# Kernel tuning notes

Measured on AMD Instinct MI355X. Metric: run time of the kernel, lower is better.

Reference implementation:

```python
import jax, jax.numpy as jnp
import numpy as np

Q7_MAX = 127.0  # int8 symmetric quant range
EPS = 1e-8


def setup_inputs() -> dict:
    key = jax.random.key(0)
    k0, k1, k2, k3 = jax.random.split(key, 4)
    tokens, d_in, d_out = 4096, 4096, 6144  # 32*128 + 8*128 + 8*128
    x = jax.random.normal(k0, (tokens, d_in), dtype=jnp.float32)
    # pre-quantized int8 weight [out_features, in_features]
    weight = jax.random.randint(k1, (d_out, d_in), -128, 128, dtype=jnp.int8)
    # per-output-channel dequant scale [out_features, 1]
    scale = jax.random.uniform(k2, (d_out, 1), dtype=jnp.float32, minval=1e-3, maxval=1e-2)
    bias = jax.random.normal(k3, (d_out,), dtype=jnp.float32) * 0.01
    return {"x": x, "weight": weight, "scale": scale, "bias": bias}


def reference(x, weight, scale, bias):
    # dynamic per-token symmetric int8 quantization of activations
    amax = jnp.max(jnp.abs(x), axis=-1, keepdims=True)          # [T, 1]
    s_x = jnp.maximum(amax, EPS) / Q7_MAX                        # per-token scale
    x_q = jnp.clip(jnp.round(x / s_x), -128.0, 127.0).astype(jnp.int8)
    acc = jnp.matmul(x_q.astype(jnp.int32), weight.astype(jnp.int32).T)
    # fused dequant: per-token act scale * per-channel weight scale, plus bias
    out = acc.astype(jnp.float32) * s_x * scale.T + bias
    return out
```

## Files before the change

kernel.cpp:

```cpp
#include <hip/hip_runtime.h>
#include <stdint.h>
#include <stddef.h>

typedef __attribute__((ext_vector_type(4))) int i32x4;

#define AS1q __attribute__((address_space(1)))
#define AS3q __attribute__((address_space(3)))

__device__ __forceinline__ void gload16(const void* g, void* l) {
    __builtin_amdgcn_global_load_lds((const AS1q uint32_t*)g, (AS3q uint32_t*)l, 16, 0, 0);
}

#define VMCNT0()  asm volatile("s_waitcnt vmcnt(0)" ::: "memory")
#define BARRIER() asm volatile("s_barrier" ::: "memory")
#define SB()      __builtin_amdgcn_sched_barrier(0)
#define SP1()     __builtin_amdgcn_s_setprio(1)
#define SP0()     __builtin_amdgcn_s_setprio(0)
#define MFMAI8(a, b, c) __builtin_amdgcn_mfma_i32_16x16x64_i8(a, b, c, 0, 0, 0)

#define EPSQ 1e-8f

__global__ __launch_bounds__(256) void quant4096(
    const float* __restrict__ x, int8_t* __restrict__ xq, float* __restrict__ sx)
{
    constexpr int K = 4096;
    const int t = blockIdx.x;
    const int tid = threadIdx.x;
    const float4* row4 = (const float4*)(x + (size_t)t * K);
    float4 v0 = row4[0 * 256 + tid];
    float4 v1 = row4[1 * 256 + tid];
    float4 v2 = row4[2 * 256 + tid];
    float4 v3 = row4[3 * 256 + tid];
    auto mx4 = [](float4 a) {
        return fmaxf(fmaxf(fabsf(a.x), fabsf(a.y)), fmaxf(fabsf(a.z), fabsf(a.w)));
    };
    float am = fmaxf(fmaxf(mx4(v0), mx4(v1)), fmaxf(mx4(v2), mx4(v3)));
    #pragma unroll
    for (int off = 32; off > 0; off >>= 1)
        am = fmaxf(am, __shfl_xor(am, off, 64));
    __shared__ float wmax[4];
    if ((tid & 63) == 0) wmax[tid >> 6] = am;
    __syncthreads();
    float r = fmaxf(fmaxf(wmax[0], wmax[1]), fmaxf(wmax[2], wmax[3]));
    const float s = fmaxf(r, EPSQ) / 127.0f;
    if (tid == 0) sx[t] = s;
    int* qrow = (int*)(xq + (size_t)t * K);
    auto pack = [&](float4 a) {
        int q0 = (int)fminf(fmaxf(rintf(a.x / s), -128.f), 127.f);
        int q1 = (int)fminf(fmaxf(rintf(a.y / s), -128.f), 127.f);
        int q2 = (int)fminf(fmaxf(rintf(a.z / s), -128.f), 127.f);
        int q3 = (int)fminf(fmaxf(rintf(a.w / s), -128.f), 127.f);
        return (q0 & 255) | ((q1 & 255) << 8) | ((q2 & 255) << 16) | ((q3 & 255) << 24);
    };
    qrow[0 * 256 + tid] = pack(v0);
    qrow[1 * 256 + tid] = pack(v1);
    qrow[2 * 256 + tid] = pack(v2);
    qrow[3 * 256 + tid] = pack(v3);
}

__global__ __launch_bounds__(256) void quant_any(
    const float* __restrict__ x, int8_t* __restrict__ xq, float* __restrict__ sx, int K)
{
    const int t = blockIdx.x;
    const int tid = threadIdx.x;
    const float* row = x + (size_t)t * K;
    float am = 0.f;
    for (int i = tid; i < K; i += 256) am = fmaxf(am, fabsf(row[i]));
    #pragma unroll
    for (int off = 32; off > 0; off >>= 1)
        am = fmaxf(am, __shfl_xor(am, off, 64));
    __shared__ float wmax[4];
    if ((tid & 63) == 0) wmax[tid >> 6] = am;
    __syncthreads();
    float r = fmaxf(fmaxf(wmax[0], wmax[1]), fmaxf(wmax[2], wmax[3]));
    const float s = fmaxf(r, EPSQ) / 127.0f;
    if (tid == 0) sx[t] = s;
    int8_t* qrow = xq + (size_t)t * K;
    for (int i = tid; i < K; i += 256) {
        float q = fminf(fmaxf(rintf(row[i] / s), -128.f), 127.f);
        qrow[i] = (int8_t)(int)q;
    }
}

__global__ __launch_bounds__(256) void pack_w(
    const int* __restrict__ w32, int8_t* __restrict__ w8, long long n4)
{
    const long long stride = (long long)gridDim.x * 256;
    for (long long i = (long long)blockIdx.x * 256 + threadIdx.x; i < n4; i += stride) {
        int4 v = ((const int4*)w32)[i];
        ((int*)w8)[i] = (v.x & 255) | ((v.y & 255) << 8) | ((v.z & 255) << 16) | ((v.w & 255) << 24);
    }
}

__global__ __launch_bounds__(512, 2) void gemm_i8(
    const int8_t* __restrict__ xq, const int8_t* __restrict__ w,
    const float* __restrict__ sx, const float* __restrict__ scale,
    const float* __restrict__ bias, float* __restrict__ out,
    int M, int N, int K)
{
    __shared__ __align__(16) uint8_t lds[2][57344];
    const int tid  = threadIdx.x;
    const int lane = tid & 63;
    const int wv   = tid >> 6;
    const int wr   = wv >> 2, wc = wv & 3;

    const int nwg = gridDim.x;
    const int q8 = nwg >> 3, r8 = nwg & 7;
    const int xcd = blockIdx.x & 7, idx8 = blockIdx.x >> 3;
    const int wg = (xcd < r8 ? xcd * (q8 + 1) : r8 * (q8 + 1) + (xcd - r8) * q8) + idx8;

    const int NBM = M >> 8;
    const int bm = wg % NBM;
    const int bn = wg / NBM;
    const int brow = bm << 8, bcol = bn * 192;

    const int8_t* srcA[4];
    #pragma unroll
    for (int e = 0; e < 4; ++e) {
        int half = e >> 1;
        int li = (e & 1) * 512 + tid;
        int R  = li >> 3;
        int xx = ((li & 7) << 4) ^ ((R & 7) << 4);
        srcA[e] = xq + (size_t)(brow + ((R << 1) | (xx >> 6))) * K + half * 64 + (xx & 63);
    }
    const int8_t* srcB[3];
    #pragma unroll
    for (int e = 0; e < 3; ++e) {
        int li = e * 512 + tid;
        int halfB = (li >= 768) ? 1 : 0;
        int lw = li - halfB * 768;
        int R  = lw >> 3;
        int xx = ((li & 7) << 4) ^ ((R & 7) << 4);
        srcB[e] = w + (size_t)(bcol + ((R << 1) | (xx >> 6))) * K + halfB * 64 + (xx & 63);
    }

    int offA[8], offB[3];
    #pragma unroll
    for (int m = 0; m < 8; ++m) {
        int r  = wr * 128 + m * 16 + (lane & 15);
        int R  = r >> 1;
        int x  = (((r & 1) << 6) | (lane & 48)) ^ ((R & 7) << 4);
        offA[m] = R * 128 + x;
    }
    #pragma unroll
    for (int n = 0; n < 3; ++n) {
        int r  = wc * 48 + n * 16 + (lane & 15);
        int R  = r >> 1;
        int x  = (((r & 1) << 6) | (lane & 48)) ^ ((R & 7) << 4);
        offB[n] = R * 128 + x;
    }

    i32x4 acc[8][3] = {};

#define STAGE(NB, TT) do { const size_t ko = (size_t)(TT) << 7;      \
        gload16(srcA[0] + ko, &lds[NB][        wv * 1024]);          \
        gload16(srcA[1] + ko, &lds[NB][ 8192 + wv * 1024]);          \
        gload16(srcA[2] + ko, &lds[NB][16384 + wv * 1024]);          \
        gload16(srcA[3] + ko, &lds[NB][24576 + wv * 1024]);          \
        gload16(srcB[0] + ko, &lds[NB][32768 + wv * 1024]);          \
        gload16(srcB[1] + ko, &lds[NB][40960 + wv * 1024]);          \
        gload16(srcB[2] + ko, &lds[NB][49152 + wv * 1024]); } while (0)

#define RA(BUF, HH, V, MM) V = *(const i32x4*)(&lds[BUF][(HH) * 16384 + offA[MM]])
#define RB(BUF, HH, V, NN) V = *(const i32x4*)(&lds[BUF][32768 + (HH) * 12288 + offB[NN]])

#define TILE(BUF, TT, DOSTAGE) do {                                           \
        i32x4 a0,a1,a2,a3,a4,a5,a6,a7,b0,b1,b2;                               \
        i32x4 c0,c1,c2,c3,c4,c5,c6,c7,d0,d1,d2;                               \
        VMCNT0(); BARRIER(); SB();                                            \
        RA(BUF,0,a0,0); RA(BUF,0,a1,1); RB(BUF,0,b0,0); RB(BUF,0,b1,1); SB(); \
        RA(BUF,0,a2,2); RA(BUF,0,a3,3); RB(BUF,0,b2,2); SB();                 \
        RA(BUF,0,a4,4); RA(BUF,0,a5,5); RA(BUF,0,a6,6); RA(BUF,0,a7,7); SB(); \
        if (DOSTAGE) { STAGE(BUF ^ 1, (TT) + 1); }                            \
        SB();                                                                 \
        SP1();                                                                \
        acc[0][0]=MFMAI8(a0,b0,acc[0][0]); acc[1][0]=MFMAI8(a1,b0,acc[1][0]); \
        acc[0][1]=MFMAI8(a0,b1,acc[0][1]); acc[1][1]=MFMAI8(a1,b1,acc[1][1]); \
        SP0(); SB();                                                          \
        RA(BUF,1,c0,0); RA(BUF,1,c1,1); RB(BUF,1,d0,0); RB(BUF,1,d1,1); SB(); \
        SP1();                                                                \
        acc[0][2]=MFMAI8(a0,b2,acc[0][2]); acc[1][2]=MFMAI8(a1,b2,acc[1][2]); \
        acc[2][0]=MFMAI8(a2,b0,acc[2][0]); acc[3][0]=MFMAI8(a3,b0,acc[3][0]); \
        acc[2][1]=MFMAI8(a2,b1,acc[2][1]); acc[3][1]=MFMAI8(a3,b1,acc[3][1]); \
        acc[2][2]=MFMAI8(a2,b2,acc[2][2]); acc[3][2]=MFMAI8(a3,b2,acc[3][2]); \
        SP0(); SB();                                                          \
        RA(BUF,1,c2,2); RA(BUF,1,c3,3); RB(BUF,1,d2,2); SB();                 \
        SP1();                                                                \
        acc[4][0]=MFMAI8(a4,b0,acc[4][0]); acc[5][0]=MFMAI8(a5,b0,acc[5][0]); \
        acc[6][0]=MFMAI8(a6,b0,acc[6][0]); acc[7][0]=MFMAI8(a7,b0,acc[7][0]); \
        acc[4][1]=MFMAI8(a4,b1,acc[4][1]); acc[5][1]=MFMAI8(a5,b1,acc[5][1]); \
        acc[6][1]=MFMAI8(a6,b1,acc[6][1]); acc[7][1]=MFMAI8(a7,b1,acc[7][1]); \
        acc[4][2]=MFMAI8(a4,b2,acc[4][2]); acc[5][2]=MFMAI8(a5,b2,acc[5][2]); \
        acc[6][2]=MFMAI8(a6,b2,acc[6][2]); acc[7][2]=MFMAI8(a7,b2,acc[7][2]); \
        SP0(); SB();                                                          \
        RA(BUF,1,c4,4); RA(BUF,1,c5,5); RA(BUF,1,c6,6); RA(BUF,1,c7,7); SB(); \
        SP1();                                                                \
        acc[0][0]=MFMAI8(c0,d0,acc[0][0]); acc[1][0]=MFMAI8(c1,d0,acc[1][0]); \
        acc[0][1]=MFMAI8(c0,d1,acc[0][1]); acc[1][1]=MFMAI8(c1,d1,acc[1][1]); \
        acc[0][2]=MFMAI8(c0,d2,acc[0][2]); acc[1][2]=MFMAI8(c1,d2,acc[1][2]); \
        acc[2][0]=MFMAI8(c2,d0,acc[2][0]); acc[3][0]=MFMAI8(c3,d0,acc[3][0]); \
        acc[2][1]=MFMAI8(c2,d1,acc[2][1]); acc[3][1]=MFMAI8(c3,d1,acc[3][1]); \
        acc[2][2]=MFMAI8(c2,d2,acc[2][2]); acc[3][2]=MFMAI8(c3,d2,acc[3][2]); \
        acc[4][0]=MFMAI8(c4,d0,acc[4][0]); acc[5][0]=MFMAI8(c5,d0,acc[5][0]); \
        acc[6][0]=MFMAI8(c6,d0,acc[6][0]); acc[7][0]=MFMAI8(c7,d0,acc[7][0]); \
        acc[4][1]=MFMAI8(c4,d1,acc[4][1]); acc[5][1]=MFMAI8(c5,d1,acc[5][1]); \
        acc[6][1]=MFMAI8(c6,d1,acc[6][1]); acc[7][1]=MFMAI8(c7,d1,acc[7][1]); \
        acc[4][2]=MFMAI8(c4,d2,acc[4][2]); acc[5][2]=MFMAI8(c5,d2,acc[5][2]); \
        acc[6][2]=MFMAI8(c6,d2,acc[6][2]); acc[7][2]=MFMAI8(c7,d2,acc[7][2]); \
        SP0(); SB();                                                          \
    } while (0)

    const int NT = K >> 7;
    STAGE(0, 0);
    for (int t = 0; t < NT - 2; t += 2) {
        TILE(0, t,     true);
        TILE(1, t + 1, true);
    }
    TILE(0, NT - 2, true);
    TILE(1, NT - 1, false);

    const int orow = brow + wr * 128;
    const int ocol = bcol + wc * 48;
    float sxv[8][4];
    #pragma unroll
    for (int m = 0; m < 8; ++m)
        #pragma unroll
        for (int j = 0; j < 4; ++j)
            sxv[m][j] = sx[orow + m * 16 + ((lane >> 4) << 2) + j];
    #pragma unroll
    for (int n = 0; n < 3; ++n) {
        const int col = ocol + n * 16 + (lane & 15);
        const float sc = scale[col];
        const float bi = bias[col];
        #pragma unroll
        for (int m = 0; m < 8; ++m) {
            const int rb = orow + m * 16 + ((lane >> 4) << 2);
            #pragma unroll
            for (int j = 0; j < 4; ++j)
                out[(size_t)(rb + j) * N + col] = (float)acc[m][n][j] * sxv[m][j] * sc + bi;
        }
    }
}

extern "C" void kernel_launch(void* const* d_in, const int* in_sizes, int n_in,
                              void* d_out, int out_size, void* d_ws, size_t ws_size,
                              hipStream_t stream) {
    const float* x     = (const float*)d_in[0];
    const int*   w32   = (const int*)d_in[1];
    const float* scale = (const float*)d_in[2];
    const float* bias  = (const float*)d_in[3];
    float* out = (float*)d_out;

    const int N = in_sizes[2];
    const int K = in_sizes[1] / N;
    const int M = in_sizes[0] / K;

    int8_t* xqbuf = (int8_t*)d_ws;
    int8_t* wqbuf = (int8_t*)d_ws + (size_t)M * K;
    float*  sxbuf = (float*)((uint8_t*)d_ws + (size_t)M * K + (size_t)N * K);

    if (K == 4096)
        quant4096<<<M, 256, 0, stream>>>(x, xqbuf, sxbuf);
    else
        quant_any<<<M, 256, 0, stream>>>(x, xqbuf, sxbuf, K);

    pack_w<<<2048, 256, 0, stream>>>(w32, wqbuf, (long long)N * K / 4);

    const int nwg = (M / 256) * (N / 192);
    gemm_i8<<<nwg, 512, 0, stream>>>(xqbuf, wqbuf, sxbuf, scale, bias, out, M, N, K);
}
```

Before: 142.1 us.

## Triple-buffer A tiles and use partial vmcnt waits to deepen the prefetch

Splits the shared LDS buffer into separate A and B regions: A gets three slots, B keeps two. Each iteration waits with vmcnt(4) instead of vmcnt(0), then issues the B load for the next tile and the A load two tiles ahead, both before the LDS reads of the current tile. The aim is to hide more global-load latency behind the MFMA work and avoid draining every outstanding load at each barrier. In exchange, LDS use per block rises to about 144 KB, and the pipeline prologue and epilogue get more special cases.

```diff
diff --git a/kernel.cpp b/kernel.cpp
--- a/kernel.cpp
+++ b/kernel.cpp
@@ -11,6 +11,7 @@
     __builtin_amdgcn_global_load_lds((const AS1q uint32_t*)g, (AS3q uint32_t*)l, 16, 0, 0);
 }
 
+#define VMCNT4()  asm volatile("s_waitcnt vmcnt(4)" ::: "memory")
 #define VMCNT0()  asm volatile("s_waitcnt vmcnt(0)" ::: "memory")
 #define BARRIER() asm volatile("s_barrier" ::: "memory")
 #define SB()      __builtin_amdgcn_sched_barrier(0)
@@ -98,7 +99,8 @@
     const float* __restrict__ bias, float* __restrict__ out,
     int M, int N, int K)
 {
-    __shared__ __align__(16) uint8_t lds[2][57344];
+    __shared__ __align__(16) uint8_t ldsA[3][32768];
+    __shared__ __align__(16) uint8_t ldsB[2][24576];
     const int tid  = threadIdx.x;
     const int lane = tid & 63;
     const int wv   = tid >> 6;
@@ -152,39 +154,37 @@
 
     i32x4 acc[8][3] = {};
 
-#define STAGE(NB, TT) do { const size_t ko = (size_t)(TT) << 7;      \
-        gload16(srcA[0] + ko, &lds[NB][        wv * 1024]);          \
-        gload16(srcA[1] + ko, &lds[NB][ 8192 + wv * 1024]);          \
-        gload16(srcA[2] + ko, &lds[NB][16384 + wv * 1024]);          \
-        gload16(srcA[3] + ko, &lds[NB][24576 + wv * 1024]);          \
-        gload16(srcB[0] + ko, &lds[NB][32768 + wv * 1024]);          \
-        gload16(srcB[1] + ko, &lds[NB][40960 + wv * 1024]);          \
-        gload16(srcB[2] + ko, &lds[NB][49152 + wv * 1024]); } while (0)
-
-#define RA(BUF, HH, V, MM) V = *(const i32x4*)(&lds[BUF][(HH) * 16384 + offA[MM]])
-#define RB(BUF, HH, V, NN) V = *(const i32x4*)(&lds[BUF][32768 + (HH) * 12288 + offB[NN]])
-
-#define TILE(BUF, TT, DOSTAGE) do {                                           \
+#define STAGE_A(DST, TT) do { const size_t ko = (size_t)(TT) << 7;   \
+        gload16(srcA[0] + ko, (DST) +         wv * 1024);            \
+        gload16(srcA[1] + ko, (DST) +  8192 + wv * 1024);            \
+        gload16(srcA[2] + ko, (DST) + 16384 + wv * 1024);            \
+        gload16(srcA[3] + ko, (DST) + 24576 + wv * 1024); } while (0)
+#define STAGE_B(DST, TT) do { const size_t ko = (size_t)(TT) << 7;   \
+        gload16(srcB[0] + ko, (DST) +         wv * 1024);            \
+        gload16(srcB[1] + ko, (DST) +  8192 + wv * 1024);            \
+        gload16(srcB[2] + ko, (DST) + 16384 + wv * 1024); } while (0)
+
+#define RA(BA, HH, V, MM) V = *(const i32x4*)((BA) + (HH) * 16384 + offA[MM])
+#define RB(BB, HH, V, NN) V = *(const i32x4*)((BB) + (HH) * 12288 + offB[NN])
+
+#define TILE_BODY(BA, BB) do {                                                \
         i32x4 a0,a1,a2,a3,a4,a5,a6,a7,b0,b1,b2;                               \
         i32x4 c0,c1,c2,c3,c4,c5,c6,c7,d0,d1,d2;                               \
-        VMCNT0(); BARRIER(); SB();                                            \
-        RA(BUF,0,a0,0); RA(BUF,0,a1,1); RB(BUF,0,b0,0); RB(BUF,0,b1,1); SB(); \
-        RA(BUF,0,a2,2); RA(BUF,0,a3,3); RB(BUF,0,b2,2); SB();                 \
-        RA(BUF,0,a4,4); RA(BUF,0,a5,5); RA(BUF,0,a6,6); RA(BUF,0,a7,7); SB(); \
-        if (DOSTAGE) { STAGE(BUF ^ 1, (TT) + 1); }                            \
-        SB();                                                                 \
+        RA(BA,0,a0,0); RA(BA,0,a1,1); RB(BB,0,b0,0); RB(BB,0,b1,1); SB();     \
+        RA(BA,0,a2,2); RA(BA,0,a3,3); RB(BB,0,b2,2); SB();                    \
+        RA(BA,0,a4,4); RA(BA,0,a5,5); RA(BA,0,a6,6); RA(BA,0,a7,7); SB();     \
         SP1();                                                                \
         acc[0][0]=MFMAI8(a0,b0,acc[0][0]); acc[1][0]=MFMAI8(a1,b0,acc[1][0]); \
         acc[0][1]=MFMAI8(a0,b1,acc[0][1]); acc[1][1]=MFMAI8(a1,b1,acc[1][1]); \
         SP0(); SB();                                                          \
-        RA(BUF,1,c0,0); RA(BUF,1,c1,1); RB(BUF,1,d0,0); RB(BUF,1,d1,1); SB(); \
+        RA(BA,1,c0,0); RA(BA,1,c1,1); RB(BB,1,d0,0); RB(BB,1,d1,1); SB();     \
         SP1();                                                                \
         acc[0][2]=MFMAI8(a0,b2,acc[0][2]); acc[1][2]=MFMAI8(a1,b2,acc[1][2]); \
         acc[2][0]=MFMAI8(a2,b0,acc[2][0]); acc[3][0]=MFMAI8(a3,b0,acc[3][0]); \
         acc[2][1]=MFMAI8(a2,b1,acc[2][1]); acc[3][1]=MFMAI8(a3,b1,acc[3][1]); \
         acc[2][2]=MFMAI8(a2,b2,acc[2][2]); acc[3][2]=MFMAI8(a3,b2,acc[3][2]); \
         SP0(); SB();                                                          \
-        RA(BUF,1,c2,2); RA(BUF,1,c3,3); RB(BUF,1,d2,2); SB();                 \
+        RA(BA,1,c2,2); RA(BA,1,c3,3); RB(BB,1,d2,2); SB();                    \
         SP1();                                                                \
         acc[4][0]=MFMAI8(a4,b0,acc[4][0]); acc[5][0]=MFMAI8(a5,b0,acc[5][0]); \
         acc[6][0]=MFMAI8(a6,b0,acc[6][0]); acc[7][0]=MFMAI8(a7,b0,acc[7][0]); \
@@ -193,7 +193,7 @@
         acc[4][2]=MFMAI8(a4,b2,acc[4][2]); acc[5][2]=MFMAI8(a5,b2,acc[5][2]); \
         acc[6][2]=MFMAI8(a6,b2,acc[6][2]); acc[7][2]=MFMAI8(a7,b2,acc[7][2]); \
         SP0(); SB();                                                          \
-        RA(BUF,1,c4,4); RA(BUF,1,c5,5); RA(BUF,1,c6,6); RA(BUF,1,c7,7); SB(); \
+        RA(BA,1,c4,4); RA(BA,1,c5,5); RA(BA,1,c6,6); RA(BA,1,c7,7); SB();     \
         SP1();                                                                \
         acc[0][0]=MFMAI8(c0,d0,acc[0][0]); acc[1][0]=MFMAI8(c1,d0,acc[1][0]); \
         acc[0][1]=MFMAI8(c0,d1,acc[0][1]); acc[1][1]=MFMAI8(c1,d1,acc[1][1]); \
@@ -211,13 +211,37 @@
     } while (0)
 
     const int NT = K >> 7;
-    STAGE(0, 0);
-    for (int t = 0; t < NT - 2; t += 2) {
-        TILE(0, t,     true);
-        TILE(1, t + 1, true);
-    }
-    TILE(0, NT - 2, true);
-    TILE(1, NT - 1, false);
+    STAGE_A(&ldsA[0][0], 0);
+    STAGE_B(&ldsB[0][0], 0);
+    STAGE_A(&ldsA[1][0], 1);
+
+    int ia = 0;
+    for (int t = 0; t < NT - 2; ++t) {
+        uint8_t* bA = &ldsA[ia][0];
+        uint8_t* bB = &ldsB[t & 1][0];
+        int ia2 = ia + 2; if (ia2 >= 3) ia2 -= 3;
+        VMCNT4(); BARRIER(); SB();
+        STAGE_B(&ldsB[(t & 1) ^ 1][0], t + 1);
+        STAGE_A(&ldsA[ia2][0], t + 2);
+        SB();
+        TILE_BODY(bA, bB);
+        ia = (ia == 2) ? 0 : ia + 1;
+    }
+    {
+        uint8_t* bA = &ldsA[ia][0];
+        uint8_t* bB = &ldsB[(NT - 2) & 1][0];
+        VMCNT4(); BARRIER(); SB();
+        STAGE_B(&ldsB[(NT - 1) & 1][0], NT - 1);
+        SB();
+        TILE_BODY(bA, bB);
+        ia = (ia == 2) ? 0 : ia + 1;
+    }
+    {
+        uint8_t* bA = &ldsA[ia][0];
+        uint8_t* bB = &ldsB[(NT - 1) & 1][0];
+        VMCNT0(); BARRIER(); SB();
+        TILE_BODY(bA, bB);
+    }
 
     const int orow = brow + wr * 128;
     const int ocol = bcol + wc * 48;
```

Measured after the change: 176.0 us. 23.8% more time.

## Switch GEMM inner loop to 32x32x32 int8 MFMA with 4x2 wave grid

Applied to the files above, without the earlier changes.

Replaces the 16x16x64 int8 MFMA with the 32x32x32 variant and changes the wave layout from 2x4 to 4x2. Each wave now computes a 64x96 sub-tile as 2x3 fragments of 32x32. The LDS read offsets and the epilogue row mapping are rewritten to match the new fragment layout. The goal is fewer LDS fragment reads per MFMA FLOP and higher per-instruction throughput, at the cost of a different LDS access pattern that may hit bank conflicts against the existing swizzle.

```diff
diff --git a/kernel.cpp b/kernel.cpp
--- a/kernel.cpp
+++ b/kernel.cpp
@@ -2,7 +2,8 @@
 #include <stdint.h>
 #include <stddef.h>
 
-typedef __attribute__((ext_vector_type(4))) int i32x4;
+typedef __attribute__((ext_vector_type(4)))  int i32x4;
+typedef __attribute__((ext_vector_type(16))) int i32x16;
 
 #define AS1q __attribute__((address_space(1)))
 #define AS3q __attribute__((address_space(3)))
@@ -16,7 +17,7 @@
 #define SB()      __builtin_amdgcn_sched_barrier(0)
 #define SP1()     __builtin_amdgcn_s_setprio(1)
 #define SP0()     __builtin_amdgcn_s_setprio(0)
-#define MFMAI8(a, b, c) __builtin_amdgcn_mfma_i32_16x16x64_i8(a, b, c, 0, 0, 0)
+#define MFMA32(a, b, c) __builtin_amdgcn_mfma_i32_32x32x32_i8(a, b, c, 0, 0, 0)
 
 #define EPSQ 1e-8f
 
@@ -102,7 +103,7 @@
     const int tid  = threadIdx.x;
     const int lane = tid & 63;
     const int wv   = tid >> 6;
-    const int wr   = wv >> 2, wc = wv & 3;
+    const int wr   = wv >> 1, wc = wv & 1;
 
     const int nwg = gridDim.x;
     const int q8 = nwg >> 3, r8 = nwg & 7;
@@ -134,23 +135,29 @@
         srcB[e] = w + (size_t)(bcol + ((R << 1) | (xx >> 6))) * K + halfB * 64 + (xx & 63);
     }
 
-    int offA[8], offB[3];
-    #pragma unroll
-    for (int m = 0; m < 8; ++m) {
-        int r  = wr * 128 + m * 16 + (lane & 15);
-        int R  = r >> 1;
-        int x  = (((r & 1) << 6) | (lane & 48)) ^ ((R & 7) << 4);
-        offA[m] = R * 128 + x;
-    }
-    #pragma unroll
-    for (int n = 0; n < 3; ++n) {
-        int r  = wc * 48 + n * 16 + (lane & 15);
-        int R  = r >> 1;
-        int x  = (((r & 1) << 6) | (lane & 48)) ^ ((R & 7) << 4);
-        offB[n] = R * 128 + x;
-    }
-
-    i32x4 acc[8][3] = {};
+    int offA[2][2], offB[3][2];
+    #pragma unroll
+    for (int f = 0; f < 2; ++f)
+        #pragma unroll
+        for (int s = 0; s < 2; ++s) {
+            int r = wr * 64 + f * 32 + (lane & 31);
+            int c = s * 32 + ((lane >> 5) << 4);
+            int R = r >> 1;
+            int x = (((r & 1) << 6) | c) ^ ((R & 7) << 4);
+            offA[f][s] = R * 128 + x;
+        }
+    #pragma unroll
+    for (int g = 0; g < 3; ++g)
+        #pragma unroll
+        for (int s = 0; s < 2; ++s) {
+            int r = wc * 96 + g * 32 + (lane & 31);
+            int c = s * 32 + ((lane >> 5) << 4);
+            int R = r >> 1;
+            int x = (((r & 1) << 6) | c) ^ ((R & 7) << 4);
+            offB[g][s] = R * 128 + x;
+        }
+
+    i32x16 acc[2][3] = {};
 
 #define STAGE(NB, TT) do { const size_t ko = (size_t)(TT) << 7;      \
         gload16(srcA[0] + ko, &lds[NB][        wv * 1024]);          \
@@ -161,53 +168,37 @@
         gload16(srcB[1] + ko, &lds[NB][40960 + wv * 1024]);          \
         gload16(srcB[2] + ko, &lds[NB][49152 + wv * 1024]); } while (0)
 
-#define RA(BUF, HH, V, MM) V = *(const i32x4*)(&lds[BUF][(HH) * 16384 + offA[MM]])
-#define RB(BUF, HH, V, NN) V = *(const i32x4*)(&lds[BUF][32768 + (HH) * 12288 + offB[NN]])
+#define RA(BUF, HH, V, FF, SS) V = *(const i32x4*)(&lds[BUF][(HH) * 16384 + offA[FF][SS]])
+#define RB(BUF, HH, V, GG, SS) V = *(const i32x4*)(&lds[BUF][32768 + (HH) * 12288 + offB[GG][SS]])
+
+#define KSTEP(X0, X1, Y0, Y1, Y2)                                   \
+    SP1();                                                          \
+    acc[0][0] = MFMA32(X0, Y0, acc[0][0]);                          \
+    acc[1][0] = MFMA32(X1, Y0, acc[1][0]);                          \
+    acc[0][1] = MFMA32(X0, Y1, acc[0][1]);                          \
+    acc[1][1] = MFMA32(X1, Y1, acc[1][1]);                          \
+    acc[0][2] = MFMA32(X0, Y2, acc[0][2]);                          \
+    acc[1][2] = MFMA32(X1, Y2, acc[1][2]);                          \
+    SP0();
 
 #define TILE(BUF, TT, DOSTAGE) do {                                           \
-        i32x4 a0,a1,a2,a3,a4,a5,a6,a7,b0,b1,b2;                               \
-        i32x4 c0,c1,c2,c3,c4,c5,c6,c7,d0,d1,d2;                               \
+        i32x4 a00,a10,b00,b10,b20, a01,a11,b01,b11,b21;                       \
+        i32x4 c00,c10,d00,d10,d20, c01,c11,d01,d11,d21;                       \
         VMCNT0(); BARRIER(); SB();                                            \
-        RA(BUF,0,a0,0); RA(BUF,0,a1,1); RB(BUF,0,b0,0); RB(BUF,0,b1,1); SB(); \
-        RA(BUF,0,a2,2); RA(BUF,0,a3,3); RB(BUF,0,b2,2); SB();                 \
-        RA(BUF,0,a4,4); RA(BUF,0,a5,5); RA(BUF,0,a6,6); RA(BUF,0,a7,7); SB(); \
+        RA(BUF,0,a00,0,0); RA(BUF,0,a10,1,0);                                 \
+        RB(BUF,0,b00,0,0); RB(BUF,0,b10,1,0); RB(BUF,0,b20,2,0); SB();        \
+        RA(BUF,0,a01,0,1); RA(BUF,0,a11,1,1);                                 \
+        RB(BUF,0,b01,0,1); RB(BUF,0,b11,1,1); RB(BUF,0,b21,2,1); SB();        \
         if (DOSTAGE) { STAGE(BUF ^ 1, (TT) + 1); }                            \
         SB();                                                                 \
-        SP1();                                                                \
-        acc[0][0]=MFMAI8(a0,b0,acc[0][0]); acc[1][0]=MFMAI8(a1,b0,acc[1][0]); \
-        acc[0][1]=MFMAI8(a0,b1,acc[0][1]); acc[1][1]=MFMAI8(a1,b1,acc[1][1]); \
-        SP0(); SB();                                                          \
-        RA(BUF,1,c0,0); RA(BUF,1,c1,1); RB(BUF,1,d0,0); RB(BUF,1,d1,1); SB(); \
-        SP1();                                                                \
-        acc[0][2]=MFMAI8(a0,b2,acc[0][2]); acc[1][2]=MFMAI8(a1,b2,acc[1][2]); \
-        acc[2][0]=MFMAI8(a2,b0,acc[2][0]); acc[3][0]=MFMAI8(a3,b0,acc[3][0]); \
-        acc[2][1]=MFMAI8(a2,b1,acc[2][1]); acc[3][1]=MFMAI8(a3,b1,acc[3][1]); \
-        acc[2][2]=MFMAI8(a2,b2,acc[2][2]); acc[3][2]=MFMAI8(a3,b2,acc[3][2]); \
-        SP0(); SB();                                                          \
-        RA(BUF,1,c2,2); RA(BUF,1,c3,3); RB(BUF,1,d2,2); SB();                 \
-        SP1();                                                                \
-        acc[4][0]=MFMAI8(a4,b0,acc[4][0]); acc[5][0]=MFMAI8(a5,b0,acc[5][0]); \
-        acc[6][0]=MFMAI8(a6,b0,acc[6][0]); acc[7][0]=MFMAI8(a7,b0,acc[7][0]); \
-        acc[4][1]=MFMAI8(a4,b1,acc[4][1]); acc[5][1]=MFMAI8(a5,b1,acc[5][1]); \
-        acc[6][1]=MFMAI8(a6,b1,acc[6][1]); acc[7][1]=MFMAI8(a7,b1,acc[7][1]); \
-        acc[4][2]=MFMAI8(a4,b2,acc[4][2]); acc[5][2]=MFMAI8(a5,b2,acc[5][2]); \
-        acc[6][2]=MFMAI8(a6,b2,acc[6][2]); acc[7][2]=MFMAI8(a7,b2,acc[7][2]); \
-        SP0(); SB();                                                          \
-        RA(BUF,1,c4,4); RA(BUF,1,c5,5); RA(BUF,1,c6,6); RA(BUF,1,c7,7); SB(); \
-        SP1();                                                                \
-        acc[0][0]=MFMAI8(c0,d0,acc[0][0]); acc[1][0]=MFMAI8(c1,d0,acc[1][0]); \
-        acc[0][1]=MFMAI8(c0,d1,acc[0][1]); acc[1][1]=MFMAI8(c1,d1,acc[1][1]); \
-        acc[0][2]=MFMAI8(c0,d2,acc[0][2]); acc[1][2]=MFMAI8(c1,d2,acc[1][2]); \
-        acc[2][0]=MFMAI8(c2,d0,acc[2][0]); acc[3][0]=MFMAI8(c3,d0,acc[3][0]); \
-        acc[2][1]=MFMAI8(c2,d1,acc[2][1]); acc[3][1]=MFMAI8(c3,d1,acc[3][1]); \
-        acc[2][2]=MFMAI8(c2,d2,acc[2][2]); acc[3][2]=MFMAI8(c3,d2,acc[3][2]); \
-        acc[4][0]=MFMAI8(c4,d0,acc[4][0]); acc[5][0]=MFMAI8(c5,d0,acc[5][0]); \
-        acc[6][0]=MFMAI8(c6,d0,acc[6][0]); acc[7][0]=MFMAI8(c7,d0,acc[7][0]); \
-        acc[4][1]=MFMAI8(c4,d1,acc[4][1]); acc[5][1]=MFMAI8(c5,d1,acc[5][1]); \
-        acc[6][1]=MFMAI8(c6,d1,acc[6][1]); acc[7][1]=MFMAI8(c7,d1,acc[7][1]); \
-        acc[4][2]=MFMAI8(c4,d2,acc[4][2]); acc[5][2]=MFMAI8(c5,d2,acc[5][2]); \
-        acc[6][2]=MFMAI8(c6,d2,acc[6][2]); acc[7][2]=MFMAI8(c7,d2,acc[7][2]); \
-        SP0(); SB();                                                          \
+        KSTEP(a00, a10, b00, b10, b20); SB();                                 \
+        RA(BUF,1,c00,0,0); RA(BUF,1,c10,1,0);                                 \
+        RB(BUF,1,d00,0,0); RB(BUF,1,d10,1,0); RB(BUF,1,d20,2,0); SB();        \
+        KSTEP(a01, a11, b01, b11, b21); SB();                                 \
+        RA(BUF,1,c01,0,1); RA(BUF,1,c11,1,1);                                 \
+        RB(BUF,1,d01,0,1); RB(BUF,1,d11,1,1); RB(BUF,1,d21,2,1); SB();        \
+        KSTEP(c00, c10, d00, d10, d20); SB();                                 \
+        KSTEP(c01, c11, d01, d11, d21); SB();                                 \
     } while (0)
 
     const int NT = K >> 7;
@@ -219,25 +210,28 @@
     TILE(0, NT - 2, true);
     TILE(1, NT - 1, false);
 
-    const int orow = brow + wr * 128;
-    const int ocol = bcol + wc * 48;
-    float sxv[8][4];
-    #pragma unroll
-    for (int m = 0; m < 8; ++m)
-        #pragma unroll
-        for (int j = 0; j < 4; ++j)
-            sxv[m][j] = sx[orow + m * 16 + ((lane >> 4) << 2) + j];
-    #pragma unroll
-    for (int n = 0; n < 3; ++n) {
-        const int col = ocol + n * 16 + (lane & 15);
+    const int orow = brow + wr * 64;
+    const int ocol = bcol + wc * 96;
+    const int rlo  = (lane >> 5) << 2;
+    float sxv[2][16];
+    #pragma unroll
+    for (int f = 0; f < 2; ++f)
+        #pragma unroll
+        for (int r = 0; r < 16; ++r)
+            sxv[f][r] = sx[orow + f * 32 + (r & 3) + ((r >> 2) << 3) + rlo];
+    #pragma unroll
+    for (int g = 0; g < 3; ++g) {
+        const int col = ocol + g * 32 + (lane & 31);
         const float sc = scale[col];
         const float bi = bias[col];
         #pragma unroll
-        for (int m = 0; m < 8; ++m) {
-            const int rb = orow + m * 16 + ((lane >> 4) << 2);
+        for (int f = 0; f < 2; ++f) {
+            const int rb = orow + f * 32 + rlo;
             #pragma unroll
-            for (int j = 0; j < 4; ++j)
-                out[(size_t)(rb + j) * N + col] = (float)acc[m][n][j] * sxv[m][j] * sc + bi;
+            for (int r = 0; r < 16; ++r) {
+                const int row = rb + (r & 3) + ((r >> 2) << 3);
+                out[(size_t)row * N + col] = (float)acc[f][g][r] * sxv[f][r] * sc + bi;
+            }
         }
     }
 }
```

After: 151.4 us. 1.07x slower.
